# Performance work log

Measured on AMD Instinct MI355X. Metric: run time of the kernel, lower is better.

Reference implementation:

```python
import jax, jax.numpy as jnp
import numpy as np

N_STOCKS = 5
SPD_DIM = N_STOCKS * (N_STOCKS + 1) // 2  # 15
STATE_DIM = N_STOCKS * N_STOCKS           # 25
CTX_DIM = 64
HIDDEN = 128
N_STEPS = 5
DT = 0.2
DIFFUSION_SCALE = 1.0
B = 4096
T = 32


def _spd_basis(n):
    bs = []
    for i in range(n):
        e = np.zeros((n, n), np.float32); e[i, i] = 1.0; bs.append(e)
    for i in range(n):
        for j in range(i + 1, n):
            e = np.zeros((n, n), np.float32)
            e[i, j] = e[j, i] = 1.0 / np.sqrt(2.0)
            bs.append(e)
    return jnp.asarray(np.stack(bs))  # (d, n, n) orthonormal symmetric basis

BASIS = _spd_basis(N_STOCKS)


def _sym(x):
    return 0.5 * (x + jnp.swapaxes(x, -1, -2))


def setup_inputs() -> dict:
    key = jax.random.key(0)
    ks = jax.random.split(key, 20)
    S, C, H, D = STATE_DIM, CTX_DIM, HIDDEN, SPD_DIM
    raw = jax.random.normal(ks[0], (B, T, N_STOCKS, N_STOCKS), jnp.float32)
    context_spd = raw @ jnp.swapaxes(raw, -1, -2) / N_STOCKS + jnp.eye(N_STOCKS, dtype=jnp.float32)
    dW = jax.random.normal(ks[1], (B, N_STEPS, D), jnp.float32) * jnp.sqrt(DT).astype(jnp.float32)

    def lin(k, out_d, in_d, scale=1.0):
        return jax.random.normal(k, (out_d, in_d), jnp.float32) * (scale / np.sqrt(in_d))

    inp_d = S + C  # 89
    return {
        "context_spd": context_spd,
        "dW": dW,
        "gru_wih": lin(ks[2], 3 * H, S),
        "gru_whh": lin(ks[3], 3 * H, H),
        "gru_bias": jnp.zeros((3 * H,), jnp.float32),
        "gru_bias_n": jnp.zeros((H,), jnp.float32),
        "proj_w": lin(ks[4], C, H),
        "proj_b": jnp.zeros((C,), jnp.float32),
        "drift_w0": lin(ks[5], H, inp_d), "drift_b0": jnp.zeros((H,), jnp.float32),
        "drift_w1": lin(ks[6], H, H),    "drift_b1": jnp.zeros((H,), jnp.float32),
        "drift_w2": lin(ks[7], H, H),    "drift_b2": jnp.zeros((H,), jnp.float32),
        "drift_w3": lin(ks[8], D, H) * 0.001, "drift_b3": jnp.zeros((D,), jnp.float32),
        "diff_w0": lin(ks[9], H, inp_d), "diff_b0": jnp.zeros((H,), jnp.float32),
        "diff_w1": lin(ks[10], H, H),   "diff_b1": jnp.zeros((H,), jnp.float32),
        "diff_w2": lin(ks[11], D, H) * 0.001, "diff_b2": jnp.full((D,), -3.0, jnp.float32),
    }


def reference(context_spd, dW, gru_wih, gru_whh, gru_bias, gru_bias_n, proj_w, proj_b,
              drift_w0, drift_b0, drift_w1, drift_b1, drift_w2, drift_b2, drift_w3, drift_b3,
              diff_w0, diff_b0, diff_w1, diff_b1, diff_w2, diff_b2):
    b = context_spd.shape[0]
    n = context_spd.shape[-1]

    # ---- GRU encoder over flattened symmetrized SPD matrices ----
    feats = _sym(context_spd).reshape(b, context_spd.shape[1], n * n)  # (B, T, S)

    def gru_step(h, x):  # x: (B, S), h: (B, H)
        gi = x @ gru_wih.T + gru_bias
        gh = h @ gru_whh.T
        ir, iz, ig = jnp.split(gi, 3, axis=-1)
        hr, hz, hg = jnp.split(gh, 3, axis=-1)
        r = jax.nn.sigmoid(ir + hr)
        z = jax.nn.sigmoid(iz + hz)
        g = jnp.tanh(ig + r * (hg + gru_bias_n))
        return (1.0 - z) * g + z * h, None

    h0 = jnp.zeros((b, gru_whh.shape[1]), feats.dtype)
    hT, _ = jax.lax.scan(gru_step, h0, jnp.swapaxes(feats, 0, 1))
    ctx = hT @ proj_w.T + proj_b  # (B, ctx_dim)

    # ---- SPD geometry helpers (affine-invariant frame) ----
    def sqrtm_sym(sig):
        w, v = jnp.linalg.eigh(sig)
        w = jnp.clip(w, 1e-8, None)
        return (v * jnp.sqrt(w)[..., None, :]) @ jnp.swapaxes(v, -1, -2)

    def expm_sym(a):
        w, v = jnp.linalg.eigh(a)
        return (v * jnp.exp(w)[..., None, :]) @ jnp.swapaxes(v, -1, -2)

    # ---- geometric Euler-Maruyama SDE step ----
    def sde_step(sigma, dw):  # sigma: (B,n,n), dw: (B,d)
        state = _sym(sigma).reshape(b, -1)
        inp = jnp.concatenate([state, ctx], axis=-1)  # (B, 89)
        # drift MLP (depth 3: 4 linears, silu)
        h = jax.nn.silu(inp @ drift_w0.T + drift_b0)
        h = jax.nn.silu(h @ drift_w1.T + drift_b1)
        h = jax.nn.silu(h @ drift_w2.T + drift_b2)
        drift_c = h @ drift_w3.T + drift_b3  # (B, d)
        # diffusion MLP (depth 2: 3 linears, silu), softplus-scaled
        g = jax.nn.silu(inp @ diff_w0.T + diff_b0)
        g = jax.nn.silu(g @ diff_w1.T + diff_b1)
        scales = jax.nn.softplus(g @ diff_w2.T + diff_b2) * DIFFUSION_SCALE  # (B, d)
        coeff = drift_c * DT + scales * dw  # tangent coordinates in orthonormal frame
        a = jnp.einsum('bk,kij->bij', coeff, BASIS)  # symmetric (B,n,n)
        L = sqrtm_sym(_sym(sigma))  # symmetric sqrt; frame E_k = L B_k L
        sigma_new = L @ expm_sym(a) @ L  # exp map: L expm(L^-1 V L^-1) L
        return _sym(sigma_new), None

    y0 = _sym(context_spd[:, -1])
    yT, _ = jax.lax.scan(sde_step, y0, jnp.swapaxes(dW, 0, 1))
    return _sym(yT)
```

## Files before the change

### kernel.cpp

```cpp
#include <hip/hip_runtime.h>
#include <hip/hip_bf16.h>

typedef unsigned int uint;

#define T_STEPS 32

#define OFF_WB    0
#define OFF_PJB   30720
#define OFF_D0B   34816
#define OFF_D1B   40960
#define OFF_D2B   49152
#define OFF_G0B   57344
#define OFF_G1B   63488
#define OFF_W3B   71680
#define OFF_G2B   72704

typedef _Float16 half8 __attribute__((ext_vector_type(8)));
typedef float    f32x4 __attribute__((ext_vector_type(4)));

union FB { uint4 u4; half8 h; };

__device__ inline uint pack2f(float a, float b) {
  _Float16 ha = (_Float16)a, hb = (_Float16)b;
  unsigned short ua, ub;
  __builtin_memcpy(&ua, &ha, 2);
  __builtin_memcpy(&ub, &hb, 2);
  return (uint)ua | ((uint)ub << 16);
}

__device__ inline float sigm(float x) { return 1.f / (1.f + __expf(-x)); }
__device__ inline float tanh_f(float x) {
  float ax = fabsf(x);
  float e = __expf(2.f * ax);
  float t = 1.f - 2.f / (e + 1.f);
  return copysignf(t, x);
}
__device__ inline float silu_f(float x) { return x / (1.f + __expf(-x)); }

__device__ inline float map89(const float* __restrict__ W, int u, int k) {
  if (k < 25) return W[u * 89 + k];
  if (k < 32) return 0.f;
  return W[u * 89 + k - 7];
}

__global__ __launch_bounds__(256) void prep_kernel(
    const float* __restrict__ wih, const float* __restrict__ whh,
    const float* __restrict__ pw,
    const float* __restrict__ dw0, const float* __restrict__ dw1,
    const float* __restrict__ dw2, const float* __restrict__ gw0,
    const float* __restrict__ gw1, const float* __restrict__ dw3,
    const float* __restrict__ gw2, uint* __restrict__ wsu) {
  int id = blockIdx.x * 256 + threadIdx.x;
  if (id < 30720) {
    int i = id & 3, l = (id >> 2) & 63, t3 = id >> 8;
    int kt = t3 % 5, wg = t3 / 5;
    int w = wg / 3, gi = wg % 3;
    int row = gi * 128 + w * 16 + (l & 15);
    int k = ((l >> 4) << 3) + i * 2;
    float a, b;
    if (kt == 0) {
      a = (k     < 25) ? wih[row * 25 + k]     : 0.f;
      b = (k + 1 < 25) ? wih[row * 25 + k + 1] : 0.f;
    } else {
      int kh = (kt - 1) * 32 + k;
      a = whh[row * 128 + kh];
      b = whh[row * 128 + kh + 1];
    }
    wsu[OFF_WB + id] = pack2f(a, b);
  } else if (id < 34816) {
    int t = id - 30720;
    int i = t & 3, l = (t >> 2) & 63, wkt = t >> 8;
    int kt = wkt & 3, w = wkt >> 2;
    int u = w * 16 + (l & 15);
    int k = kt * 32 + ((l >> 4) << 3) + i * 2;
    wsu[OFF_PJB + t] = pack2f(pw[u * 128 + k], pw[u * 128 + k + 1]);
  } else if (id < 40960) {
    int t = id - 34816;
    int i = t & 3, l = (t >> 2) & 63, wkt = t >> 8;
    int kt = wkt % 3, w = wkt / 3;
    int u = w * 16 + (l & 15);
    int k = kt * 32 + ((l >> 4) << 3) + i * 2;
    wsu[OFF_D0B + t] = pack2f(map89(dw0, u, k), map89(dw0, u, k + 1));
  } else if (id < 49152) {
    int t = id - 40960;
    int i = t & 3, l = (t >> 2) & 63, wkt = t >> 8;
    int kt = wkt & 3, w = wkt >> 2;
    int u = w * 16 + (l & 15);
    int k = kt * 32 + ((l >> 4) << 3) + i * 2;
    wsu[OFF_D1B + t] = pack2f(dw1[u * 128 + k], dw1[u * 128 + k + 1]);
  } else if (id < 57344) {
    int t = id - 49152;
    int i = t & 3, l = (t >> 2) & 63, wkt = t >> 8;
    int kt = wkt & 3, w = wkt >> 2;
    int u = w * 16 + (l & 15);
    int k = kt * 32 + ((l >> 4) << 3) + i * 2;
    wsu[OFF_D2B + t] = pack2f(dw2[u * 128 + k], dw2[u * 128 + k + 1]);
  } else if (id < 63488) {
    int t = id - 57344;
    int i = t & 3, l = (t >> 2) & 63, wkt = t >> 8;
    int kt = wkt % 3, w = wkt / 3;
    int u = w * 16 + (l & 15);
    int k = kt * 32 + ((l >> 4) << 3) + i * 2;
    wsu[OFF_G0B + t] = pack2f(map89(gw0, u, k), map89(gw0, u, k + 1));
  } else if (id < 71680) {
    int t = id - 63488;
    int i = t & 3, l = (t >> 2) & 63, wkt = t >> 8;
    int kt = wkt & 3, w = wkt >> 2;
    int u = w * 16 + (l & 15);
    int k = kt * 32 + ((l >> 4) << 3) + i * 2;
    wsu[OFF_G1B + t] = pack2f(gw1[u * 128 + k], gw1[u * 128 + k + 1]);
  } else if (id < 72704) {
    int t = id - 71680;
    int i = t & 3, l = (t >> 2) & 63, kt = t >> 8;
    int o = l & 15;
    int k = kt * 32 + ((l >> 4) << 3) + i * 2;
    float a = (o < 15) ? dw3[o * 128 + k]     : 0.f;
    float b = (o < 15) ? dw3[o * 128 + k + 1] : 0.f;
    wsu[OFF_W3B + t] = pack2f(a, b);
  } else if (id < 73728) {
    int t = id - 72704;
    int i = t & 3, l = (t >> 2) & 63, kt = t >> 8;
    int o = l & 15;
    int k = kt * 32 + ((l >> 4) << 3) + i * 2;
    float a = (o < 15) ? gw2[o * 128 + k]     : 0.f;
    float b = (o < 15) ? gw2[o * 128 + k + 1] : 0.f;
    wsu[OFF_G2B + t] = pack2f(a, b);
  }
}

template <int KT>
__device__ inline void mlp_pair(const _Float16* __restrict__ aA,
                                const FB* B0, const FB* B1,
                                float bias0, float bias1,
                                _Float16* __restrict__ outA,
                                int lm, int lq, int ubase) {
  f32x4 c0 = {0.f, 0.f, 0.f, 0.f}, c1 = {0.f, 0.f, 0.f, 0.f};
#pragma unroll
  for (int kt = 0; kt < KT; kt++) {
    half8 a = *(const half8*)(aA + ((kt * 4 + lq) * 16 + lm) * 8);
    c0 = __builtin_amdgcn_mfma_f32_16x16x32_f16(a, B0[kt].h, c0, 0, 0, 0);
    c1 = __builtin_amdgcn_mfma_f32_16x16x32_f16(a, B1[kt].h, c1, 0, 0, 0);
  }
  int u0 = ubase + lm, u1 = ubase + 16 + lm;
  int base0 = (u0 >> 3) * 128 + (u0 & 7);
  int base1 = (u1 >> 3) * 128 + (u1 & 7);
#pragma unroll
  for (int s = 0; s < 4; s++) {
    outA[base0 + (lq * 4 + s) * 8] = (_Float16)silu_f(c0[s] + bias0);
    outA[base1 + (lq * 4 + s) * 8] = (_Float16)silu_f(c1[s] + bias1);
  }
}

__device__ inline f32x4 head4(const _Float16* __restrict__ aA, const FB* H,
                              int lm, int lq) {
  f32x4 c = {0.f, 0.f, 0.f, 0.f};
#pragma unroll
  for (int kt = 0; kt < 4; kt++) {
    half8 a = *(const half8*)(aA + ((kt * 4 + lq) * 16 + lm) * 8);
    c = __builtin_amdgcn_mfma_f32_16x16x32_f16(a, H[kt].h, c, 0, 0, 0);
  }
  return c;
}

__device__ inline float mm5(float A, float Bv, int i, int j) {
  float c = 0.f;
#pragma unroll
  for (int k = 0; k < 5; k++)
    c = fmaf(__shfl(A, i * 5 + k, 32), __shfl(Bv, k * 5 + j, 32), c);
  return c;
}

#define NS_ITER do { \
  float P_  = mm5(Zv, Yv, gii, gjj); \
  float Tm_ = 1.5f * gdel - 0.5f * P_; \
  float Yn_ = mm5(Yv, Tm_, gii, gjj); \
  float Zn_ = mm5(Tm_, Zv, gii, gjj); \
  Yv = Yn_; Zv = Zn_; } while (0)

__global__ __launch_bounds__(512) void fused_kernel(
    const float* __restrict__ ctp, const float* __restrict__ dWp,
    const uint* __restrict__ wsu,
    const float* __restrict__ gbias, const float* __restrict__ gbn,
    const float* __restrict__ projb,
    const float* __restrict__ db0, const float* __restrict__ db1,
    const float* __restrict__ db2, const float* __restrict__ b3,
    const float* __restrict__ gb0, const float* __restrict__ gb1,
    const float* __restrict__ gb2, float* __restrict__ outp) {
  __shared__ __align__(16) _Float16 bigbuf[16384];
  __shared__ __align__(16) _Float16 hf[2][4][4][16][8];
  __shared__ float sig_s[16 * 28];
  __shared__ float coeff_s[256];
  __shared__ float coeff2_s[256];
  const int tid = threadIdx.x;
  const int rb = blockIdx.x * 16;
  uint* bigu = (uint*)bigbuf;

  for (int idx = tid; idx < T_STEPS * 16 * 16; idx += 512) {
    int k2 = idx & 15, r = (idx >> 4) & 15, t = idx >> 8;
    const float* base = ctp + ((rb + r) * T_STEPS + t) * 25;
    int k0 = 2 * k2;
    float v0 = 0.f, v1 = 0.f;
    if (k0 < 25)     { int i5 = k0 / 5,     j5 = k0 % 5;     v0 = 0.5f * (base[i5*5+j5] + base[j5*5+i5]); }
    if (k0 + 1 < 25) { int i5 = (k0+1) / 5, j5 = (k0+1) % 5; v1 = 0.5f * (base[i5*5+j5] + base[j5*5+i5]); }
    int q = k2 >> 2, jh = k2 & 3;
    bigu[((t * 4 + q) * 16 + r) * 4 + jh] = pack2f(v0, v1);
  }

  const int w = tid >> 6, l = tid & 63;
  const int lm = l & 15, lq = l >> 4;
  const int u = w * 16 + lm;
  const int ku = u >> 5, qu = (u >> 3) & 3, ju = u & 7;
  FB Bf[3][5];
  const uint4* wb4p = (const uint4*)(wsu + OFF_WB);
#pragma unroll
  for (int gi = 0; gi < 3; gi++)
#pragma unroll
    for (int kt = 0; kt < 5; kt++)
      Bf[gi][kt].u4 = wb4p[((w * 3 + gi) * 5 + kt) * 64 + l];
  const float br = gbias[u], bz = gbias[128 + u], bg = gbias[256 + u], bn = gbn[u];
  float hprev[4] = {0.f, 0.f, 0.f, 0.f};
  __syncthreads();

  f32x4 z4 = {0.f, 0.f, 0.f, 0.f};
  half8 axn = *(const half8*)(bigbuf + ((0 * 4 + lq) * 16 + lm) * 8);
  f32x4 pxr = __builtin_amdgcn_mfma_f32_16x16x32_f16(axn, Bf[0][0].h, z4, 0, 0, 0);
  f32x4 pxz = __builtin_amdgcn_mfma_f32_16x16x32_f16(axn, Bf[1][0].h, z4, 0, 0, 0);
  f32x4 pxg = __builtin_amdgcn_mfma_f32_16x16x32_f16(axn, Bf[2][0].h, z4, 0, 0, 0);
  for (int t = 0; t < T_STEPS; t++) {
    f32x4 cr = pxr, cz = pxz, cgv = pxg;
    f32x4 ch = {0.f, 0.f, 0.f, 0.f};
    if (t > 0) {
      const int p = t & 1;
#pragma unroll
      for (int kk = 0; kk < 4; kk++) {
        half8 ah = *(const half8*)(&hf[p][kk][lq][lm][0]);
        cr = __builtin_amdgcn_mfma_f32_16x16x32_f16(ah, Bf[0][1 + kk].h, cr, 0, 0, 0);
        cz = __builtin_amdgcn_mfma_f32_16x16x32_f16(ah, Bf[1][1 + kk].h, cz, 0, 0, 0);
        ch = __builtin_amdgcn_mfma_f32_16x16x32_f16(ah, Bf[2][1 + kk].h, ch, 0, 0, 0);
      }
    }
    if (t < T_STEPS - 1) {
      axn = *(const half8*)(bigbuf + (((t + 1) * 4 + lq) * 16 + lm) * 8);
      pxr = __builtin_amdgcn_mfma_f32_16x16x32_f16(axn, Bf[0][0].h, z4, 0, 0, 0);
      pxz = __builtin_amdgcn_mfma_f32_16x16x32_f16(axn, Bf[1][0].h, z4, 0, 0, 0);
      pxg = __builtin_amdgcn_mfma_f32_16x16x32_f16(axn, Bf[2][0].h, z4, 0, 0, 0);
    }
    const int wp = (t + 1) & 1;
#pragma unroll
    for (int s = 0; s < 4; s++) {
      float r = sigm(cr[s] + br);
      float z = sigm(cz[s] + bz);
      float g = tanh_f(cgv[s] + bg + r * (ch[s] + bn));
      float hn = (1.f - z) * g + z * hprev[s];
      hprev[s] = hn;
      hf[wp][ku][qu][lq * 4 + s][ju] = (_Float16)hn;
    }
    __syncthreads();
  }

  const int role = w >> 2;
  const int wbq = w & 3;
  FB F0[2][3], F1[2][4], F2[2][4], Pf[4], Hf[4];
  {
    const uint4* p0 = (const uint4*)(wsu + (role ? OFF_G0B : OFF_D0B));
    const uint4* p1 = (const uint4*)(wsu + (role ? OFF_G1B : OFF_D1B));
    const uint4* p2 = (const uint4*)(wsu + (role ? OFF_G1B : OFF_D2B));
#pragma unroll
    for (int s = 0; s < 2; s++) {
      int slot = wbq * 2 + s;
#pragma unroll
      for (int kt = 0; kt < 3; kt++) F0[s][kt].u4 = p0[(slot * 3 + kt) * 64 + l];
#pragma unroll
      for (int kt = 0; kt < 4; kt++) {
        F1[s][kt].u4 = p1[(slot * 4 + kt) * 64 + l];
        F2[s][kt].u4 = p2[(slot * 4 + kt) * 64 + l];
      }
    }
  }
  if (w < 4) {
#pragma unroll
    for (int kt = 0; kt < 4; kt++)
      Pf[kt].u4 = ((const uint4*)(wsu + OFF_PJB))[(w * 4 + kt) * 64 + l];
  }
  if (w == 0) {
#pragma unroll
    for (int kt = 0; kt < 4; kt++)
      Hf[kt].u4 = ((const uint4*)(wsu + OFF_W3B))[kt * 64 + l];
  } else if (w == 4) {
#pragma unroll
    for (int kt = 0; kt < 4; kt++)
      Hf[kt].u4 = ((const uint4*)(wsu + OFF_G2B))[kt * 64 + l];
  }
  float b0s[2], b1s[2], b2s[2];
#pragma unroll
  for (int s = 0; s < 2; s++) {
    int us = wbq * 32 + s * 16 + lm;
    b0s[s] = role ? gb0[us] : db0[us];
    b1s[s] = role ? gb1[us] : db1[us];
    b2s[s] = role ? 0.f : db2[us];
  }
  const int oc = (lm < 15) ? lm : 0;
  const float hb = (w == 0) ? b3[oc] : ((w == 4) ? gb2[oc] : 0.f);

  _Float16* inpA = bigbuf;
  _Float16* bufA = bigbuf + 1536;
  _Float16* bufB = bigbuf + 3584;
  _Float16* bufC = bigbuf + 5632;
  _Float16* bufD = bigbuf + 7680;

  if (w < 4) {
    f32x4 c = {0.f, 0.f, 0.f, 0.f};
#pragma unroll
    for (int kt = 0; kt < 4; kt++) {
      half8 a = *(const half8*)(&hf[0][kt][lq][lm][0]);
      c = __builtin_amdgcn_mfma_f32_16x16x32_f16(a, Pf[kt].h, c, 0, 0, 0);
    }
    const float pbv = projb[u];
    int kk = 32 + u, base = (kk >> 3) * 128 + (kk & 7);
#pragma unroll
    for (int s = 0; s < 4; s++)
      inpA[base + (lq * 4 + s) * 8] = (_Float16)(c[s] + pbv);
  }
  for (int idx = tid; idx < 400; idx += 512) {
    int e = idx / 25, k = idx % 25;
    int i5 = k / 5, j5 = k % 5;
    const float* base = ctp + ((rb + e) * T_STEPS + 31) * 25;
    float v = 0.5f * (base[i5 * 5 + j5] + base[j5 * 5 + i5]);
    sig_s[e * 28 + k] = v;
    inpA[(k >> 3) * 128 + e * 8 + (k & 7)] = (_Float16)v;
  }
  if (tid < 112) {
    int e = tid / 7, p = 25 + tid % 7;
    inpA[(p >> 3) * 128 + e * 8 + (p & 7)] = (_Float16)0.f;
  }
  const int ge = tid >> 5, glane = tid & 31;
  const int gli = (glane < 25) ? glane : 0;
  const int gii = gli / 5, gjj = gli % 5;
  const float gdel = (gii == gjj) ? 1.f : 0.f;
  __syncthreads();

  for (int st = 0; st < 5; st++) {
    float S = sig_s[ge * 28 + gli];
    float tr = 0.f;
#pragma unroll
    for (int d = 0; d < 5; d++) tr += __shfl(S, d * 6, 32);
    float Yv = S * (2.f / tr);
    float Zv = gdel;
    float dwv[4] = {0.f, 0.f, 0.f, 0.f};
    if (w == 4) {
#pragma unroll
      for (int s = 0; s < 4; s++)
        dwv[s] = dWp[((rb + lq * 4 + s) * 5 + st) * 15 + oc];
    }
    mlp_pair<3>(inpA, F0[0], F0[1], b0s[0], b0s[1], role ? bufB : bufA, lm, lq, wbq * 32);
    NS_ITER; NS_ITER; NS_ITER;
    __syncthreads();
    mlp_pair<4>(role ? bufB : bufA, F1[0], F1[1], b1s[0], b1s[1],
                role ? bufD : bufC, lm, lq, wbq * 32);
    NS_ITER; NS_ITER; NS_ITER;
    __syncthreads();
    if (!role) {
      mlp_pair<4>(bufC, F2[0], F2[1], b2s[0], b2s[1], bufA, lm, lq, wbq * 32);
    } else if (w == 4) {
      f32x4 c = head4(bufD, Hf, lm, lq);
      if (lm < 15) {
#pragma unroll
        for (int s = 0; s < 4; s++) {
          float acc = c[s] + hb;
          float sp = (acc > 20.f) ? acc : __logf(1.f + __expf(acc));
          coeff2_s[(lq * 4 + s) * 16 + lm] = sp * dwv[s];
        }
      }
    }
    NS_ITER; NS_ITER;
    __syncthreads();
    if (w == 0) {
      f32x4 c = head4(bufA, Hf, lm, lq);
      if (lm < 15) {
#pragma unroll
        for (int s = 0; s < 4; s++)
          coeff_s[(lq * 4 + s) * 16 + lm] = 0.2f * (c[s] + hb);
      }
    }
    NS_ITER;
    float L = Yv * sqrtf(0.5f * tr);
    __syncthreads();
    {
      float av;
      if (gii == gjj) av = coeff_s[ge * 16 + gii] + coeff2_s[ge * 16 + gii];
      else {
        int p = gii < gjj ? gii : gjj, qq = gii < gjj ? gjj : gii;
        int i5 = 5 + (p * (9 - p)) / 2 + (qq - p - 1);
        av = (coeff_s[ge * 16 + i5] + coeff2_s[ge * 16 + i5]) * 0.70710678f;
      }
      float M = gdel;
#pragma unroll
      for (int n = 7; n >= 1; n--) {
        float P = mm5(av, M, gii, gjj);
        M = gdel + P * (1.f / (float)n);
      }
      float P2 = mm5(L, M, gii, gjj);
      float S2 = mm5(P2, L, gii, gjj);
      S2 = 0.5f * (S2 + __shfl(S2, gjj * 5 + gii, 32));
      if (glane < 25) {
        sig_s[ge * 28 + gli] = S2;
        inpA[(gli >> 3) * 128 + ge * 8 + (gli & 7)] = (_Float16)S2;
      }
    }
    __syncthreads();
  }

  for (int idx = tid; idx < 400; idx += 512) {
    int e = idx / 25, k = idx % 25;
    outp[(rb + e) * 25 + k] = sig_s[e * 28 + k];
  }
}

extern "C" void kernel_launch(void* const* d_in, const int* in_sizes, int n_in,
                              void* d_out, int out_size, void* d_ws, size_t ws_size,
                              hipStream_t stream) {
  const float* ctp = (const float*)d_in[0];
  const float* dWp = (const float*)d_in[1];
  const float* wih = (const float*)d_in[2];
  const float* whh = (const float*)d_in[3];
  const float* gb  = (const float*)d_in[4];
  const float* gbn = (const float*)d_in[5];
  const float* pw  = (const float*)d_in[6];
  const float* pb  = (const float*)d_in[7];
  const float* dw0 = (const float*)d_in[8];
  const float* db0 = (const float*)d_in[9];
  const float* dw1 = (const float*)d_in[10];
  const float* db1 = (const float*)d_in[11];
  const float* dw2 = (const float*)d_in[12];
  const float* db2 = (const float*)d_in[13];
  const float* dw3 = (const float*)d_in[14];
  const float* db3 = (const float*)d_in[15];
  const float* gw0 = (const float*)d_in[16];
  const float* gb0 = (const float*)d_in[17];
  const float* gw1 = (const float*)d_in[18];
  const float* gb1 = (const float*)d_in[19];
  const float* gw2 = (const float*)d_in[20];
  const float* gb2 = (const float*)d_in[21];
  uint* wsu = (uint*)d_ws;

  hipLaunchKernelGGL(prep_kernel, dim3(288), dim3(256), 0, stream,
                     wih, whh, pw, dw0, dw1, dw2, gw0, gw1, dw3, gw2, wsu);
  hipLaunchKernelGGL(fused_kernel, dim3(256), dim3(512), 0, stream,
                     ctp, dWp, wsu, gb, gbn, pb,
                     db0, db1, db2, db3, gb0, gb1, gb2, (float*)d_out);
}
```

Baseline: 191.3 us.

## Replace Newton-Schulz iterations and Taylor expm with cheaper polynomial forms using bpermute

```diff
diff --git a/kernel.cpp b/kernel.cpp
--- a/kernel.cpp
+++ b/kernel.cpp
@@ -162,19 +162,22 @@
   return c;
 }
 
-__device__ inline float mm5(float A, float Bv, int i, int j) {
+__device__ inline float bpf(int addr, float v) {
+  return __int_as_float(__builtin_amdgcn_ds_bpermute(addr, __float_as_int(v)));
+}
+__device__ inline float mm5b(int iA, int iB, float A, float B) {
   float c = 0.f;
 #pragma unroll
   for (int k = 0; k < 5; k++)
-    c = fmaf(__shfl(A, i * 5 + k, 32), __shfl(Bv, k * 5 + j, 32), c);
+    c = fmaf(bpf(iA + 4 * k, A), bpf(iB + 20 * k, B), c);
   return c;
 }
 
 #define NS_ITER do { \
-  float P_  = mm5(Zv, Yv, gii, gjj); \
+  float P_  = mm5b(iA0, iB0, Zv, Yv); \
   float Tm_ = 1.5f * gdel - 0.5f * P_; \
-  float Yn_ = mm5(Yv, Tm_, gii, gjj); \
-  float Zn_ = mm5(Tm_, Zv, gii, gjj); \
+  float Yn_ = mm5b(iA0, iB0, Yv, Tm_); \
+  float Zn_ = mm5b(iA0, iB0, Tm_, Zv); \
   Yv = Yn_; Zv = Zn_; } while (0)
 
 __global__ __launch_bounds__(512) void fused_kernel(
@@ -337,27 +340,39 @@
   const int gli = (glane < 25) ? glane : 0;
   const int gii = gli / 5, gjj = gli % 5;
   const float gdel = (gii == gjj) ? 1.f : 0.f;
+  const int gbase = (l & 32) << 2;
+  const int iA0 = gbase + gii * 20;
+  const int iB0 = gbase + gjj * 4;
+  const int iT0 = gbase + (gjj * 5 + gii) * 4;
   __syncthreads();
 
   for (int st = 0; st < 5; st++) {
     float S = sig_s[ge * 28 + gli];
     float tr = 0.f;
 #pragma unroll
-    for (int d = 0; d < 5; d++) tr += __shfl(S, d * 6, 32);
-    float Yv = S * (2.f / tr);
-    float Zv = gdel;
+    for (int d = 0; d < 5; d++) tr += bpf(gbase + 24 * d, S);
+    const float That = S * (2.298851f / tr) - 1.068966f * gdel;
     float dwv[4] = {0.f, 0.f, 0.f, 0.f};
     if (w == 4) {
 #pragma unroll
       for (int s = 0; s < 4; s++)
         dwv[s] = dWp[((rb + lq * 4 + s) * 5 + st) * 15 + oc];
     }
+    float Yv, Zv;
     mlp_pair<3>(inpA, F0[0], F0[1], b0s[0], b0s[1], role ? bufB : bufA, lm, lq, wbq * 32);
-    NS_ITER; NS_ITER; NS_ITER;
+    {
+      float T2 = mm5b(iA0, iB0, That, That);
+      float X  = -1.13859f * That + 0.9901f * T2;
+      float Zp = mm5b(iA0, iB0, T2, X)
+               + 1.03702f * gdel - 0.21179f * That + 0.09756f * T2;
+      Zv = Zp;
+      float TZ = mm5b(iA0, iB0, That, Zp);
+      Yv = 0.87f * TZ + 0.93f * Zp;
+    }
     __syncthreads();
     mlp_pair<4>(role ? bufB : bufA, F1[0], F1[1], b1s[0], b1s[1],
                 role ? bufD : bufC, lm, lq, wbq * 32);
-    NS_ITER; NS_ITER; NS_ITER;
+    NS_ITER;
     __syncthreads();
     if (!role) {
       mlp_pair<4>(bufC, F2[0], F2[1], b2s[0], b2s[1], bufA, lm, lq, wbq * 32);
@@ -372,7 +387,7 @@
         }
       }
     }
-    NS_ITER; NS_ITER;
+    NS_ITER;
     __syncthreads();
     if (w == 0) {
       f32x4 c = head4(bufA, Hf, lm, lq);
@@ -393,15 +408,14 @@
         int i5 = 5 + (p * (9 - p)) / 2 + (qq - p - 1);
         av = (coeff_s[ge * 16 + i5] + coeff2_s[ge * 16 + i5]) * 0.70710678f;
       }
-      float M = gdel;
-#pragma unroll
-      for (int n = 7; n >= 1; n--) {
-        float P = mm5(av, M, gii, gjj);
-        M = gdel + P * (1.f / (float)n);
-      }
-      float P2 = mm5(L, M, gii, gjj);
-      float S2 = mm5(P2, L, gii, gjj);
-      S2 = 0.5f * (S2 + __shfl(S2, gjj * 5 + gii, 32));
+      float a2 = mm5b(iA0, iB0, av, av);
+      float a3 = mm5b(iA0, iB0, a2, av);
+      float q1 = gdel * 0.16666667f + av * 0.04166667f
+               + a2 * 0.00833333f + a3 * 0.00138889f;
+      float M = gdel + av + 0.5f * a2 + mm5b(iA0, iB0, a3, q1);
+      float P2 = mm5b(iA0, iB0, L, M);
+      float S2 = mm5b(iA0, iB0, P2, L);
+      S2 = 0.5f * (S2 + bpf(iT0, S2));
       if (glane < 25) {
         sig_s[ge * 28 + gli] = S2;
         inpA[(gli >> 3) * 128 + ge * 8 + (gli & 7)] = (_Float16)S2;
```

Measured after the change: 174.8 us. -8.6%, faster.
